# Performance work log

Hardware: AMD Instinct MI355X
Metric: run time of the kernel (lower is better)

## Reference

```python
import jax, jax.numpy as jnp
import numpy as np


def _scan_dir(x, A, B, reverse):
    """First-order linear recurrence h_i = A*h_{i-1} + B*x_i along last axis (W).
    x: [Bsz, C, H, W]; A, B: [C]. reverse=True scans right-to-left but returns
    states in original index order (matching torch scan_backward)."""
    xs = jnp.moveaxis(x, -1, 0)  # [W, Bsz, C, H]
    Ab = A[None, :, None]
    Bb = B[None, :, None]
    def step(h, xi):
        h = Ab * h + Bb * xi
        return h, h
    h0 = jnp.zeros_like(xs[0])
    _, hs = jax.lax.scan(step, h0, xs, reverse=reverse)
    return jnp.moveaxis(hs, 0, -1)  # [Bsz, C, H, W]


def _conv1x1(x, W, b):
    # x: [B,Cin,H,W], W: [Cout,Cin], b: [Cout]
    return jnp.einsum('bchw,dc->bdhw', x, W) + b[None, :, None, None]


def setup_inputs() -> dict:
    key = jax.random.key(0)
    ks = jax.random.split(key, 10)
    B, C, H, W = 8, 64, 128, 128
    D = 128  # hidden_dim
    return {
        'F_in': jax.random.normal(ks[0], (B, C, H, W), dtype=jnp.float32),
        'prior': jax.random.uniform(ks[1], (B, 1, H, W), dtype=jnp.float32),
        'Wi': jax.random.normal(ks[2], (D, C), dtype=jnp.float32) * 0.05,
        'bi': jnp.zeros((D,), dtype=jnp.float32),
        'A_param': jax.random.normal(ks[3], (D,), dtype=jnp.float32),
        'B_param': jax.random.normal(ks[4], (D,), dtype=jnp.float32),
        'alpha': jnp.float32(0.1),
        'gamma': jnp.float32(0.1),
        'Wf': jax.random.normal(ks[5], (D, 4 * D), dtype=jnp.float32) * 0.05,
        'bf': jnp.zeros((D,), dtype=jnp.float32),
        'Wo': jax.random.normal(ks[6], (C, D), dtype=jnp.float32) * 0.05,
        'bo': jnp.zeros((C,), dtype=jnp.float32),
    }


def reference(F_in, prior, Wi, bi, A_param, B_param, alpha, gamma, Wf, bf, Wo, bo):
    # prior has 1 channel, repeated to C channels (prior already matches HxW)
    prior_r = jnp.broadcast_to(prior, F_in.shape)
    F_mod = F_in + alpha * prior_r
    x = _conv1x1(F_mod, Wi, bi)  # [B, D, H, W]
    A = jnp.tanh(A_param)
    Bp = B_param
    h_lr = _scan_dir(x, A, Bp, reverse=False)
    h_rl = _scan_dir(x, A, Bp, reverse=True)
    xt = jnp.swapaxes(x, 2, 3)  # scan over H axis
    h_tb = jnp.swapaxes(_scan_dir(xt, A, Bp, reverse=False), 2, 3)
    h_bt = jnp.swapaxes(_scan_dir(xt, A, Bp, reverse=True), 2, 3)
    h = jnp.concatenate([h_lr, h_rl, h_tb, h_bt], axis=1)  # [B, 4D, H, W]
    h = _conv1x1(h, Wf, bf)   # fusion -> [B, D, H, W]
    out = _conv1x1(h, Wo, bo)  # output_proj -> [B, C, H, W]
    return F_mod + gamma * out
```

## Files before the change

kernel.cpp:

```cpp
#include <hip/hip_runtime.h>
#include <hip/hip_bf16.h>

typedef unsigned int u32;
typedef unsigned short u16;
typedef float f32x2 __attribute__((ext_vector_type(2)));
typedef float f32x4 __attribute__((ext_vector_type(4)));
using bf16x8 = __attribute__((ext_vector_type(8))) short;
using f32x4v = __attribute__((ext_vector_type(4))) float;

#define DEVINL __device__ __forceinline__

constexpr int XTS = 136;
constexpr int XT_BYTES = 128 * XTS * 2;
constexpr int LDS_MAIN = 2 * XT_BYTES;
constexpr int XS = 132;
constexpr int LDS_X = 128 * XS * 2;

DEVINL float bf2f(u16 u) { union { u32 i; float f; } v; v.i = ((u32)u) << 16; return v.f; }
DEVINL u16 f2bf(float f) {
  union { float f; u32 i; } v; v.f = f;
  u32 b = v.i;
  b += 0x7fffu + ((b >> 16) & 1u);
  return (u16)(b >> 16);
}
DEVINL u32 pack2(float a, float b) { return (u32)f2bf(a) | ((u32)f2bf(b) << 16); }

__global__ __launch_bounds__(256) void k_pre(
    const float* __restrict__ Wf, const float* __restrict__ Wo,
    const float* __restrict__ bf_, const float* __restrict__ bo,
    const float* __restrict__ A_param,
    float* __restrict__ A_t, float* __restrict__ beff, u16* __restrict__ Mrow) {
  const int wg = blockIdx.x, t = threadIdx.x;
  if (wg < 128) {
    const int idx = wg * 256 + t;
    const int cout = idx >> 9;
    const int k = idx & 511;
    float s = 0.f;
    for (int d = 0; d < 128; ++d) s = fmaf(Wo[cout * 128 + d], Wf[d * 512 + k], s);
    const int dir = k >> 7, dm = k & 127;
    Mrow[(dir * 64 + cout) * 128 + dm] = f2bf(s);
  } else {
    if (t < 128) A_t[t] = tanhf(A_param[t]);
    if (t < 64) {
      float s = bo[t];
      for (int d = 0; d < 128; ++d) s = fmaf(Wo[t * 128 + d], bf_[d], s);
      beff[t] = s;
    }
  }
}

extern __shared__ char smem[];

DEVINL void load_mfrags(const u16* __restrict__ Mrow, int dir_base, int lane,
                        bf16x8 (&afr)[2][4][4]) {
  const int l15 = lane & 15, kg = lane >> 4;
#pragma unroll
  for (int dir = 0; dir < 2; ++dir)
#pragma unroll
    for (int ct = 0; ct < 4; ++ct)
#pragma unroll
      for (int ks = 0; ks < 4; ++ks)
        afr[dir][ct][ks] = *(const bf16x8*)(
            Mrow + ((size_t)(dir_base + dir) * 64 + ct * 16 + l15) * 128 + ks * 32 + kg * 8);
}

template <bool REV>
DEVINL void scan_col(u16* buf, int d, float A, float Bv) {
  float hv = 0.f;
  float nx[8];
#pragma unroll
  for (int j = 0; j < 8; ++j) {
    const int idx = REV ? (127 - j) : j;
    nx[j] = bf2f(buf[idx * XTS + d]);
  }
  for (int ib = 0; ib < 128; ib += 8) {
    float cur[8];
#pragma unroll
    for (int j = 0; j < 8; ++j) cur[j] = nx[j];
    if (ib + 8 < 128) {
#pragma unroll
      for (int j = 0; j < 8; ++j) {
        const int idx = REV ? (127 - (ib + 8 + j)) : (ib + 8 + j);
        nx[j] = bf2f(buf[idx * XTS + d]);
      }
    }
#pragma unroll
    for (int j = 0; j < 8; ++j) {
      const int idx = REV ? (127 - (ib + j)) : (ib + j);
      hv = fmaf(A, hv, Bv * cur[j]);
      buf[idx * XTS + d] = f2bf(hv);
    }
  }
}

DEVINL void combine_mfma(const u16* H0, const u16* H1, const bf16x8 (&afr)[2][4][4],
                         int t, float* OutS) {
  const int lane = t & 63, wv = t >> 6;
  const int l15 = lane & 15;
  const int kgrp = (lane >> 4) * 16;
  f32x4v acc[4][2];
#pragma unroll
  for (int i = 0; i < 4; ++i)
#pragma unroll
    for (int j = 0; j < 2; ++j) acc[i][j] = (f32x4v)0.f;

#pragma unroll
  for (int dir = 0; dir < 2; ++dir) {
    const u16* Hsrc = dir ? H1 : H0;
#pragma unroll
    for (int ks = 0; ks < 4; ++ks) {
      bf16x8 bfr[2];
#pragma unroll
      for (int pt = 0; pt < 2; ++pt)
        bfr[pt] = *(const bf16x8*)((const char*)Hsrc +
                    (wv * 32 + pt * 16 + l15) * (XTS * 2) + ks * 64 + kgrp);
#pragma unroll
      for (int ct = 0; ct < 4; ++ct)
#pragma unroll
        for (int pt = 0; pt < 2; ++pt)
          acc[ct][pt] = __builtin_amdgcn_mfma_f32_16x16x32_bf16(afr[dir][ct][ks], bfr[pt], acc[ct][pt], 0, 0, 0);
    }
  }
  __syncthreads();
#pragma unroll
  for (int ct = 0; ct < 4; ++ct)
#pragma unroll
    for (int pt = 0; pt < 2; ++pt)
#pragma unroll
      for (int r = 0; r < 4; ++r)
        OutS[(ct * 16 + (lane >> 4) * 4 + r) * 134 + wv * 32 + pt * 16 + l15] = acc[ct][pt][r];
  __syncthreads();
}

__global__ __launch_bounds__(256, 2) void k_horiz(
    const float* __restrict__ F_in, const float* __restrict__ prior,
    const float* __restrict__ Wi, const float* __restrict__ bi,
    const float* __restrict__ Bp, const float* __restrict__ alpha_p,
    const float* __restrict__ A_t, const u16* __restrict__ Mrow,
    u16* __restrict__ x_out, float* __restrict__ out_partial) {
  u16* Xt = (u16*)smem;
  u16* Hl = (u16*)(smem + XT_BYTES);
  char* FT = (char*)Hl;
  float* OutS = (float*)smem;

  const int t = threadIdx.x;
  const int lane = t & 63, wv = t >> 6, l15 = lane & 15, kg = lane >> 4;
  const int bid = blockIdx.x, b = bid >> 7, h = bid & 127;

  bf16x8 bWi[8][2];
#pragma unroll
  for (int nt = 0; nt < 8; ++nt)
#pragma unroll
    for (int ks = 0; ks < 2; ++ks) {
      const float* wp = Wi + (nt * 16 + l15) * 64 + ks * 32 + kg * 8;
      const f32x4 a = *(const f32x4*)(wp);
      const f32x4 c = *(const f32x4*)(wp + 4);
      union { bf16x8 v; uint4 u; } cv;
      cv.u.x = pack2(a.x, a.y);  cv.u.y = pack2(a.z, a.w);
      cv.u.z = pack2(c.x, c.y);  cv.u.w = pack2(c.z, c.w);
      bWi[nt][ks] = cv.v;
    }

  {
    const int w = t & 127, ch = t >> 7;
    const float alpha = alpha_p[0];
    const float pv = prior[(b * 128 + h) * 128 + w];
    const float* Fb = F_in + ((size_t)b * 64 + ch * 32) * 16384 + h * 128 + w;
    const u32 sw = (u32)((w & 7) << 4);
    char* rowp = FT + w * 128;
#pragma unroll
    for (int q = 0; q < 4; ++q) {
      float fv[8];
#pragma unroll
      for (int j = 0; j < 8; ++j) fv[j] = fmaf(alpha, pv, Fb[(q * 8 + j) * 16384]);
      uint4 pk;
      pk.x = pack2(fv[0], fv[1]); pk.y = pack2(fv[2], fv[3]);
      pk.z = pack2(fv[4], fv[5]); pk.w = pack2(fv[6], fv[7]);
      *(uint4*)(rowp + ((ch * 64 + q * 16) ^ sw)) = pk;
    }
  }
  __syncthreads();

  {
    float biv[8];
#pragma unroll
    for (int nt = 0; nt < 8; ++nt) biv[nt] = bi[nt * 16 + l15];

    f32x4v acc[2][8];
#pragma unroll
    for (int i = 0; i < 2; ++i)
#pragma unroll
      for (int j = 0; j < 8; ++j) acc[i][j] = (f32x4v)0.f;

#pragma unroll
    for (int ks = 0; ks < 2; ++ks)
#pragma unroll
      for (int mt = 0; mt < 2; ++mt) {
        const int row = wv * 32 + mt * 16 + l15;
        const bf16x8 aF = *(const bf16x8*)(FT + row * 128 + ((ks * 64 + kg * 16) ^ ((row & 7) << 4)));
#pragma unroll
        for (int nt = 0; nt < 8; ++nt)
          acc[mt][nt] = __builtin_amdgcn_mfma_f32_16x16x32_bf16(aF, bWi[nt][ks], acc[mt][nt], 0, 0, 0);
      }

#pragma unroll
    for (int mt = 0; mt < 2; ++mt)
#pragma unroll
      for (int nt = 0; nt < 8; ++nt)
#pragma unroll
        for (int r = 0; r < 4; ++r) {
          const int w = wv * 32 + mt * 16 + kg * 4 + r;
          Xt[w * XTS + nt * 16 + l15] = f2bf(acc[mt][nt][r] + biv[nt]);
        }
  }
  __syncthreads();

  {
    u16* xg = x_out + (size_t)(b * 128 + h) * 16384;
    for (int i = t; i < 2048; i += 256) {
      const int r = i >> 4, q = i & 15;
      *(uint4*)(xg + r * 128 + q * 8) = *(const uint4*)((const char*)Xt + r * (XTS * 2) + q * 16);
    }
    for (int i = t; i < XT_BYTES / 16; i += 256)
      *(uint4*)((char*)Hl + i * 16) = *(const uint4*)((const char*)Xt + i * 16);
  }

  bf16x8 afr[2][4][4];
  load_mfrags(Mrow, 0, lane, afr);
  __syncthreads();

  {
    const int d = t & 127;
    const float A = A_t[d], Bv = Bp[d];
    if (t < 128) scan_col<false>(Hl, d, A, Bv);
    else         scan_col<true>(Xt, d, A, Bv);
  }
  __syncthreads();

  combine_mfma(Hl, Xt, afr, t, OutS);

  float* og = out_partial + ((size_t)b * 64 * 128 + h) * 128;
  for (int i = t; i < 8192; i += 256) {
    const int c = i >> 7, ww = i & 127;
    og[c * 16384 + ww] = OutS[c * 134 + ww];
  }
}

__global__ __launch_bounds__(256, 2) void k_vert(
    const u16* __restrict__ x_ws, const float* __restrict__ Bp,
    const float* __restrict__ A_t, const u16* __restrict__ Mrow,
    u16* __restrict__ accT) {
  u16* Xv = (u16*)smem;
  u16* Hv = (u16*)(smem + XT_BYTES);
  float* OutS = (float*)smem;

  const int t = threadIdx.x;
  const int lane = t & 63;
  const int bid = blockIdx.x, b = bid >> 7, w = bid & 127;

  for (int i = t; i < 2048; i += 256) {
    const int hh = i >> 4, q = i & 15;
    const uint4 v = *(const uint4*)(x_ws + ((size_t)(b * 128 + hh) * 128 + w) * 128 + q * 8);
    *(uint4*)((char*)Xv + hh * (XTS * 2) + q * 16) = v;
  }
  bf16x8 afr[2][4][4];
  load_mfrags(Mrow, 2, lane, afr);
  __syncthreads();
  for (int i = t; i < XT_BYTES / 16; i += 256)
    *(uint4*)((char*)Hv + i * 16) = *(const uint4*)((const char*)Xv + i * 16);
  __syncthreads();

  {
    const int d = t & 127;
    const float A = A_t[d], Bv = Bp[d];
    if (t < 128) scan_col<false>(Hv, d, A, Bv);
    else         scan_col<true>(Xv, d, A, Bv);
  }
  __syncthreads();

  combine_mfma(Hv, Xv, afr, t, OutS);

  for (int i = t; i < 4096; i += 256) {
    const int c = i >> 6, h2 = (i & 63) * 2;
    const u32 pk = pack2(OutS[c * 134 + h2], OutS[c * 134 + h2 + 1]);
    *(u32*)(accT + ((size_t)(b * 64 + c) * 128 + w) * 128 + h2) = pk;
  }
}

__global__ __launch_bounds__(256) void k_final(
    const float* __restrict__ F_in, const float* __restrict__ prior,
    const float* __restrict__ alpha_p, const float* __restrict__ gamma_p,
    const float* __restrict__ beff, const u16* __restrict__ accT,
    float* __restrict__ out) {
  u16* Xu = (u16*)smem;
  u32* Xw = (u32*)smem;
  const int t = threadIdx.x;
  const int bid = blockIdx.x, b = bid >> 6, c = bid & 63;
  const size_t base = (size_t)bid * 16384;

  for (int i = t; i < 2048; i += 256) {
    const int r = i >> 4, j = i & 15;
    const uint4 v = *(const uint4*)(accT + base + r * 128 + j * 8);
    u32* dst = Xw + r * 66 + j * 4;
    dst[0] = v.x; dst[1] = v.y; dst[2] = v.z; dst[3] = v.w;
  }
  __syncthreads();
  const float alpha = alpha_p[0], gamma = gamma_p[0];
  const float be = beff[c];
  for (int i = t; i < 2048; i += 256) {
    const int hh = i >> 4, w8 = (i & 15) * 8;
    float sv[8];
#pragma unroll
    for (int q = 0; q < 8; ++q) sv[q] = bf2f(Xu[(w8 + q) * XS + hh]);
    const size_t off = base + hh * 128 + w8;
    const float* Fp = F_in + off;
    float* Op = out + off;
    const float* Pp = prior + (b * 128 + hh) * 128 + w8;
#pragma unroll
    for (int q = 0; q < 8; ++q) {
      Op[q] = Fp[q] + alpha * Pp[q] + gamma * (Op[q] + be + sv[q]);
    }
  }
}

extern "C" void kernel_launch(void* const* d_in, const int* in_sizes, int n_in,
                              void* d_out, int out_size, void* d_ws, size_t ws_size,
                              hipStream_t stream) {
  const float* F_in   = (const float*)d_in[0];
  const float* prior  = (const float*)d_in[1];
  const float* Wi     = (const float*)d_in[2];
  const float* bi     = (const float*)d_in[3];
  const float* A_par  = (const float*)d_in[4];
  const float* B_par  = (const float*)d_in[5];
  const float* alpha  = (const float*)d_in[6];
  const float* gamma  = (const float*)d_in[7];
  const float* Wf     = (const float*)d_in[8];
  const float* bf_    = (const float*)d_in[9];
  const float* Wo     = (const float*)d_in[10];
  const float* bo     = (const float*)d_in[11];
  float* out = (float*)d_out;

  char* ws = (char*)d_ws;
  float* A_t   = (float*)ws;
  float* beff  = (float*)(ws + 512);
  u16*   Mrow  = (u16*)(ws + 1024);
  u16*   x_ws  = (u16*)(ws + 66560);
  u16*   accT  = (u16*)(ws + 66560 + 33554432);

  hipFuncSetAttribute((const void*)k_horiz, hipFuncAttributeMaxDynamicSharedMemorySize, LDS_MAIN);
  hipFuncSetAttribute((const void*)k_vert,  hipFuncAttributeMaxDynamicSharedMemorySize, LDS_MAIN);

  k_pre  <<<129, 256, 0, stream>>>(Wf, Wo, bf_, bo, A_par, A_t, beff, Mrow);
  k_horiz<<<1024, 256, LDS_MAIN, stream>>>(F_in, prior, Wi, bi, B_par, alpha, A_t, Mrow, x_ws, out);
  k_vert <<<1024, 256, LDS_MAIN, stream>>>(x_ws, B_par, A_t, Mrow, accT);
  k_final<<<512, 256, LDS_X, stream>>>(F_in, prior, alpha, gamma, beff, accT, out);
}
```

Before: 108.6 us.

## Halve LDS per block, run direction scans sequentially, store horizontal partial as bf16

The horizontal and vertical kernels now use a single LDS buffer instead of two. The forward and reverse scans run one after the other, with the source tile kept in registers and restored between passes, and each scan thread handles a channel pair packed in u32. The horizontal kernel feeds F_in straight into the MFMA A-fragments without an LDS staging pass, and folds the bias into the accumulator init. Its partial output goes to a bf16 workspace instead of fp32 in out, which k_final reads. Launch bounds rise to 4 blocks per CU, trading full-block scan parallelism (only 64 threads scan) and extra barriers for higher occupancy and less memory traffic.

Result: slower. 124.4 us (+14.6%).

```diff
diff --git a/kernel.cpp b/kernel.cpp
--- a/kernel.cpp
+++ b/kernel.cpp
@@ -12,11 +12,12 @@
 
 constexpr int XTS = 136;
 constexpr int XT_BYTES = 128 * XTS * 2;
-constexpr int LDS_MAIN = 2 * XT_BYTES;
 constexpr int XS = 132;
 constexpr int LDS_X = 128 * XS * 2;
 
 DEVINL float bf2f(u16 u) { union { u32 i; float f; } v; v.i = ((u32)u) << 16; return v.f; }
+DEVINL float bf2f_lo(u32 u) { union { u32 i; float f; } v; v.i = u << 16; return v.f; }
+DEVINL float bf2f_hi(u32 u) { union { u32 i; float f; } v; v.i = u & 0xffff0000u; return v.f; }
 DEVINL u16 f2bf(float f) {
   union { float f; u32 i; } v; v.f = f;
   u32 b = v.i;
@@ -51,96 +52,73 @@
 
 extern __shared__ char smem[];
 
-DEVINL void load_mfrags(const u16* __restrict__ Mrow, int dir_base, int lane,
-                        bf16x8 (&afr)[2][4][4]) {
-  const int l15 = lane & 15, kg = lane >> 4;
-#pragma unroll
-  for (int dir = 0; dir < 2; ++dir)
-#pragma unroll
-    for (int ct = 0; ct < 4; ++ct)
-#pragma unroll
-      for (int ks = 0; ks < 4; ++ks)
-        afr[dir][ct][ks] = *(const bf16x8*)(
-            Mrow + ((size_t)(dir_base + dir) * 64 + ct * 16 + l15) * 128 + ks * 32 + kg * 8);
-}
-
 template <bool REV>
-DEVINL void scan_col(u16* buf, int d, float A, float Bv) {
-  float hv = 0.f;
-  float nx[8];
-#pragma unroll
-  for (int j = 0; j < 8; ++j) {
-    const int idx = REV ? (127 - j) : j;
-    nx[j] = bf2f(buf[idx * XTS + d]);
-  }
+DEVINL void scan_pair(u16* buf, int dp, float A0, float A1, float B0, float B1) {
+  float h0 = 0.f, h1 = 0.f;
+  u32* base = (u32*)(buf + dp * 2);
+  constexpr int RS = XTS / 2;
+  u32 nx[8];
+#pragma unroll
+  for (int j = 0; j < 8; ++j) nx[j] = base[(REV ? (127 - j) : j) * RS];
   for (int ib = 0; ib < 128; ib += 8) {
-    float cur[8];
+    u32 cur[8];
 #pragma unroll
     for (int j = 0; j < 8; ++j) cur[j] = nx[j];
     if (ib + 8 < 128) {
 #pragma unroll
       for (int j = 0; j < 8; ++j) {
-        const int idx = REV ? (127 - (ib + 8 + j)) : (ib + 8 + j);
-        nx[j] = bf2f(buf[idx * XTS + d]);
+        const int i = ib + 8 + j;
+        nx[j] = base[(REV ? (127 - i) : i) * RS];
       }
     }
 #pragma unroll
     for (int j = 0; j < 8; ++j) {
-      const int idx = REV ? (127 - (ib + j)) : (ib + j);
-      hv = fmaf(A, hv, Bv * cur[j]);
-      buf[idx * XTS + d] = f2bf(hv);
-    }
-  }
-}
-
-DEVINL void combine_mfma(const u16* H0, const u16* H1, const bf16x8 (&afr)[2][4][4],
-                         int t, float* OutS) {
-  const int lane = t & 63, wv = t >> 6;
-  const int l15 = lane & 15;
-  const int kgrp = (lane >> 4) * 16;
-  f32x4v acc[4][2];
-#pragma unroll
-  for (int i = 0; i < 4; ++i)
-#pragma unroll
-    for (int j = 0; j < 2; ++j) acc[i][j] = (f32x4v)0.f;
-
-#pragma unroll
-  for (int dir = 0; dir < 2; ++dir) {
-    const u16* Hsrc = dir ? H1 : H0;
-#pragma unroll
-    for (int ks = 0; ks < 4; ++ks) {
-      bf16x8 bfr[2];
+      const int i = ib + j;
+      h0 = fmaf(A0, h0, B0 * bf2f_lo(cur[j]));
+      h1 = fmaf(A1, h1, B1 * bf2f_hi(cur[j]));
+      base[(REV ? (127 - i) : i) * RS] = pack2(h0, h1);
+    }
+  }
+}
+
+DEVINL void combine_pass(const u16* Hbuf, const u16* __restrict__ Mrow, int dir,
+                         int lane, int wv, f32x4v (&acc2)[4][2]) {
+  const int l15 = lane & 15, kg = lane >> 4;
+#pragma unroll
+  for (int ks = 0; ks < 4; ++ks) {
+    bf16x8 afr[4], bfr[2];
+#pragma unroll
+    for (int ct = 0; ct < 4; ++ct)
+      afr[ct] = *(const bf16x8*)(Mrow + ((size_t)dir * 64 + ct * 16 + l15) * 128 + ks * 32 + kg * 8);
+#pragma unroll
+    for (int pt = 0; pt < 2; ++pt)
+      bfr[pt] = *(const bf16x8*)((const char*)Hbuf + (wv * 32 + pt * 16 + l15) * (XTS * 2) + ks * 64 + kg * 16);
+#pragma unroll
+    for (int ct = 0; ct < 4; ++ct)
 #pragma unroll
       for (int pt = 0; pt < 2; ++pt)
-        bfr[pt] = *(const bf16x8*)((const char*)Hsrc +
-                    (wv * 32 + pt * 16 + l15) * (XTS * 2) + ks * 64 + kgrp);
-#pragma unroll
-      for (int ct = 0; ct < 4; ++ct)
-#pragma unroll
-        for (int pt = 0; pt < 2; ++pt)
-          acc[ct][pt] = __builtin_amdgcn_mfma_f32_16x16x32_bf16(afr[dir][ct][ks], bfr[pt], acc[ct][pt], 0, 0, 0);
-    }
-  }
-  __syncthreads();
+        acc2[ct][pt] = __builtin_amdgcn_mfma_f32_16x16x32_bf16(afr[ct], bfr[pt], acc2[ct][pt], 0, 0, 0);
+  }
+}
+
+DEVINL void acc_to_outs(const f32x4v (&acc2)[4][2], int lane, int wv, float* OutS) {
+  const int l15 = lane & 15, kg = lane >> 4;
 #pragma unroll
   for (int ct = 0; ct < 4; ++ct)
 #pragma unroll
     for (int pt = 0; pt < 2; ++pt)
 #pragma unroll
       for (int r = 0; r < 4; ++r)
-        OutS[(ct * 16 + (lane >> 4) * 4 + r) * 134 + wv * 32 + pt * 16 + l15] = acc[ct][pt][r];
-  __syncthreads();
-}
-
-__global__ __launch_bounds__(256, 2) void k_horiz(
+        OutS[(ct * 16 + kg * 4 + r) * 134 + wv * 32 + pt * 16 + l15] = acc2[ct][pt][r];
+}
+
+__global__ __launch_bounds__(256, 4) void k_horiz(
     const float* __restrict__ F_in, const float* __restrict__ prior,
     const float* __restrict__ Wi, const float* __restrict__ bi,
     const float* __restrict__ Bp, const float* __restrict__ alpha_p,
     const float* __restrict__ A_t, const u16* __restrict__ Mrow,
-    u16* __restrict__ x_out, float* __restrict__ out_partial) {
-  u16* Xt = (u16*)smem;
-  u16* Hl = (u16*)(smem + XT_BYTES);
-  char* FT = (char*)Hl;
+    u16* __restrict__ x_out, u16* __restrict__ Sh) {
+  u16* buf = (u16*)smem;
   float* OutS = (float*)smem;
 
   const int t = threadIdx.x;
@@ -162,128 +140,175 @@
     }
 
   {
-    const int w = t & 127, ch = t >> 7;
     const float alpha = alpha_p[0];
-    const float pv = prior[(b * 128 + h) * 128 + w];
-    const float* Fb = F_in + ((size_t)b * 64 + ch * 32) * 16384 + h * 128 + w;
-    const u32 sw = (u32)((w & 7) << 4);
-    char* rowp = FT + w * 128;
-#pragma unroll
-    for (int q = 0; q < 4; ++q) {
-      float fv[8];
-#pragma unroll
-      for (int j = 0; j < 8; ++j) fv[j] = fmaf(alpha, pv, Fb[(q * 8 + j) * 16384]);
-      uint4 pk;
-      pk.x = pack2(fv[0], fv[1]); pk.y = pack2(fv[2], fv[3]);
-      pk.z = pack2(fv[4], fv[5]); pk.w = pack2(fv[6], fv[7]);
-      *(uint4*)(rowp + ((ch * 64 + q * 16) ^ sw)) = pk;
-    }
-  }
-  __syncthreads();
-
-  {
-    float biv[8];
-#pragma unroll
-    for (int nt = 0; nt < 8; ++nt) biv[nt] = bi[nt * 16 + l15];
+    float pv[2];
+#pragma unroll
+    for (int mt = 0; mt < 2; ++mt)
+      pv[mt] = prior[(b * 128 + h) * 128 + wv * 32 + mt * 16 + l15];
 
     f32x4v acc[2][8];
 #pragma unroll
-    for (int i = 0; i < 2; ++i)
-#pragma unroll
-      for (int j = 0; j < 8; ++j) acc[i][j] = (f32x4v)0.f;
-
-#pragma unroll
-    for (int ks = 0; ks < 2; ++ks)
+    for (int mt = 0; mt < 2; ++mt)
+#pragma unroll
+      for (int nt = 0; nt < 8; ++nt) {
+        const float bv = bi[nt * 16 + l15];
+        acc[mt][nt] = (f32x4v){ bv, bv, bv, bv };
+      }
+
+#pragma unroll
+    for (int ks = 0; ks < 2; ++ks) {
+      bf16x8 aF[2];
 #pragma unroll
       for (int mt = 0; mt < 2; ++mt) {
-        const int row = wv * 32 + mt * 16 + l15;
-        const bf16x8 aF = *(const bf16x8*)(FT + row * 128 + ((ks * 64 + kg * 16) ^ ((row & 7) << 4)));
+        const int w = wv * 32 + mt * 16 + l15;
+        const float* Fp = F_in + (size_t)b * 1048576 + (size_t)(ks * 32 + kg * 8) * 16384 + h * 128 + w;
+        float fv[8];
+#pragma unroll
+        for (int j = 0; j < 8; ++j) fv[j] = fmaf(alpha, pv[mt], Fp[(size_t)j * 16384]);
+        union { bf16x8 v; uint4 u; } cv;
+        cv.u.x = pack2(fv[0], fv[1]); cv.u.y = pack2(fv[2], fv[3]);
+        cv.u.z = pack2(fv[4], fv[5]); cv.u.w = pack2(fv[6], fv[7]);
+        aF[mt] = cv.v;
+      }
+#pragma unroll
+      for (int mt = 0; mt < 2; ++mt)
 #pragma unroll
         for (int nt = 0; nt < 8; ++nt)
-          acc[mt][nt] = __builtin_amdgcn_mfma_f32_16x16x32_bf16(aF, bWi[nt][ks], acc[mt][nt], 0, 0, 0);
-      }
+          acc[mt][nt] = __builtin_amdgcn_mfma_f32_16x16x32_bf16(aF[mt], bWi[nt][ks], acc[mt][nt], 0, 0, 0);
+    }
 
 #pragma unroll
     for (int mt = 0; mt < 2; ++mt)
 #pragma unroll
       for (int nt = 0; nt < 8; ++nt)
 #pragma unroll
-        for (int r = 0; r < 4; ++r) {
-          const int w = wv * 32 + mt * 16 + kg * 4 + r;
-          Xt[w * XTS + nt * 16 + l15] = f2bf(acc[mt][nt][r] + biv[nt]);
-        }
-  }
-  __syncthreads();
-
+        for (int r = 0; r < 4; ++r)
+          buf[(wv * 32 + mt * 16 + kg * 4 + r) * XTS + nt * 16 + l15] = f2bf(acc[mt][nt][r]);
+  }
+  __syncthreads();
+
+  uint4 rld[8];
   {
     u16* xg = x_out + (size_t)(b * 128 + h) * 16384;
-    for (int i = t; i < 2048; i += 256) {
-      const int r = i >> 4, q = i & 15;
-      *(uint4*)(xg + r * 128 + q * 8) = *(const uint4*)((const char*)Xt + r * (XTS * 2) + q * 16);
-    }
-    for (int i = t; i < XT_BYTES / 16; i += 256)
-      *(uint4*)((char*)Hl + i * 16) = *(const uint4*)((const char*)Xt + i * 16);
-  }
-
-  bf16x8 afr[2][4][4];
-  load_mfrags(Mrow, 0, lane, afr);
-  __syncthreads();
-
-  {
-    const int d = t & 127;
-    const float A = A_t[d], Bv = Bp[d];
-    if (t < 128) scan_col<false>(Hl, d, A, Bv);
-    else         scan_col<true>(Xt, d, A, Bv);
-  }
-  __syncthreads();
-
-  combine_mfma(Hl, Xt, afr, t, OutS);
-
-  float* og = out_partial + ((size_t)b * 64 * 128 + h) * 128;
-  for (int i = t; i < 8192; i += 256) {
-    const int c = i >> 7, ww = i & 127;
-    og[c * 16384 + ww] = OutS[c * 134 + ww];
-  }
-}
-
-__global__ __launch_bounds__(256, 2) void k_vert(
+#pragma unroll
+    for (int j = 0; j < 8; ++j) {
+      const int i = t + j * 256;
+      rld[j] = *(const uint4*)((const char*)buf + (i >> 4) * (XTS * 2) + (i & 15) * 16);
+      *(uint4*)(xg + (i >> 4) * 128 + (i & 15) * 8) = rld[j];
+    }
+  }
+  __syncthreads();
+
+  if (t < 128 && lane < 32) {
+    const int p = wv * 32 + lane;
+    const f32x2 a = *(const f32x2*)(A_t + p * 2);
+    const f32x2 bb = *(const f32x2*)(Bp + p * 2);
+    scan_pair<false>(buf, p, a.x, a.y, bb.x, bb.y);
+  }
+  __syncthreads();
+
+  f32x4v acc2[4][2];
+#pragma unroll
+  for (int i = 0; i < 4; ++i)
+#pragma unroll
+    for (int j = 0; j < 2; ++j) acc2[i][j] = (f32x4v)0.f;
+  combine_pass(buf, Mrow, 0, lane, wv, acc2);
+  __syncthreads();
+
+#pragma unroll
+  for (int j = 0; j < 8; ++j) {
+    const int i = t + j * 256;
+    *(uint4*)((char*)buf + (i >> 4) * (XTS * 2) + (i & 15) * 16) = rld[j];
+  }
+  __syncthreads();
+
+  if (t < 128 && lane < 32) {
+    const int p = wv * 32 + lane;
+    const f32x2 a = *(const f32x2*)(A_t + p * 2);
+    const f32x2 bb = *(const f32x2*)(Bp + p * 2);
+    scan_pair<true>(buf, p, a.x, a.y, bb.x, bb.y);
+  }
+  __syncthreads();
+
+  combine_pass(buf, Mrow, 1, lane, wv, acc2);
+  __syncthreads();
+
+  acc_to_outs(acc2, lane, wv, OutS);
+  __syncthreads();
+
+  u16* sg = Sh + ((size_t)(b * 64) * 128 + h) * 128;
+  for (int i = t; i < 4096; i += 256) {
+    const int c = i >> 6, w2 = (i & 63) * 2;
+    const f32x2 v = *(const f32x2*)(OutS + c * 134 + w2);
+    *(u32*)(sg + (size_t)c * 16384 + w2) = pack2(v.x, v.y);
+  }
+}
+
+__global__ __launch_bounds__(256, 4) void k_vert(
     const u16* __restrict__ x_ws, const float* __restrict__ Bp,
     const float* __restrict__ A_t, const u16* __restrict__ Mrow,
     u16* __restrict__ accT) {
-  u16* Xv = (u16*)smem;
-  u16* Hv = (u16*)(smem + XT_BYTES);
+  u16* buf = (u16*)smem;
   float* OutS = (float*)smem;
 
   const int t = threadIdx.x;
-  const int lane = t & 63;
+  const int lane = t & 63, wv = t >> 6;
   const int bid = blockIdx.x, b = bid >> 7, w = bid & 127;
 
-  for (int i = t; i < 2048; i += 256) {
-    const int hh = i >> 4, q = i & 15;
-    const uint4 v = *(const uint4*)(x_ws + ((size_t)(b * 128 + hh) * 128 + w) * 128 + q * 8);
-    *(uint4*)((char*)Xv + hh * (XTS * 2) + q * 16) = v;
-  }
-  bf16x8 afr[2][4][4];
-  load_mfrags(Mrow, 2, lane, afr);
-  __syncthreads();
-  for (int i = t; i < XT_BYTES / 16; i += 256)
-    *(uint4*)((char*)Hv + i * 16) = *(const uint4*)((const char*)Xv + i * 16);
-  __syncthreads();
-
-  {
-    const int d = t & 127;
-    const float A = A_t[d], Bv = Bp[d];
-    if (t < 128) scan_col<false>(Hv, d, A, Bv);
-    else         scan_col<true>(Xv, d, A, Bv);
-  }
-  __syncthreads();
-
-  combine_mfma(Hv, Xv, afr, t, OutS);
+  uint4 rld[8];
+#pragma unroll
+  for (int j = 0; j < 8; ++j) {
+    const int i = t + j * 256;
+    rld[j] = *(const uint4*)(x_ws + ((size_t)(b * 128 + (i >> 4)) * 128 + w) * 128 + (i & 15) * 8);
+  }
+#pragma unroll
+  for (int j = 0; j < 8; ++j) {
+    const int i = t + j * 256;
+    *(uint4*)((char*)buf + (i >> 4) * (XTS * 2) + (i & 15) * 16) = rld[j];
+  }
+  __syncthreads();
+
+  if (t < 128 && lane < 32) {
+    const int p = wv * 32 + lane;
+    const f32x2 a = *(const f32x2*)(A_t + p * 2);
+    const f32x2 bb = *(const f32x2*)(Bp + p * 2);
+    scan_pair<false>(buf, p, a.x, a.y, bb.x, bb.y);
+  }
+  __syncthreads();
+
+  f32x4v acc2[4][2];
+#pragma unroll
+  for (int i = 0; i < 4; ++i)
+#pragma unroll
+    for (int j = 0; j < 2; ++j) acc2[i][j] = (f32x4v)0.f;
+  combine_pass(buf, Mrow, 2, lane, wv, acc2);
+  __syncthreads();
+
+#pragma unroll
+  for (int j = 0; j < 8; ++j) {
+    const int i = t + j * 256;
+    *(uint4*)((char*)buf + (i >> 4) * (XTS * 2) + (i & 15) * 16) = rld[j];
+  }
+  __syncthreads();
+
+  if (t < 128 && lane < 32) {
+    const int p = wv * 32 + lane;
+    const f32x2 a = *(const f32x2*)(A_t + p * 2);
+    const f32x2 bb = *(const f32x2*)(Bp + p * 2);
+    scan_pair<true>(buf, p, a.x, a.y, bb.x, bb.y);
+  }
+  __syncthreads();
+
+  combine_pass(buf, Mrow, 3, lane, wv, acc2);
+  __syncthreads();
+
+  acc_to_outs(acc2, lane, wv, OutS);
+  __syncthreads();
 
   for (int i = t; i < 4096; i += 256) {
     const int c = i >> 6, h2 = (i & 63) * 2;
-    const u32 pk = pack2(OutS[c * 134 + h2], OutS[c * 134 + h2 + 1]);
-    *(u32*)(accT + ((size_t)(b * 64 + c) * 128 + w) * 128 + h2) = pk;
+    const f32x2 v = *(const f32x2*)(OutS + c * 134 + h2);
+    *(u32*)(accT + ((size_t)(b * 64 + c) * 128 + w) * 128 + h2) = pack2(v.x, v.y);
   }
 }
 
@@ -291,7 +316,7 @@
     const float* __restrict__ F_in, const float* __restrict__ prior,
     const float* __restrict__ alpha_p, const float* __restrict__ gamma_p,
     const float* __restrict__ beff, const u16* __restrict__ accT,
-    float* __restrict__ out) {
+    const u16* __restrict__ Sh, float* __restrict__ out) {
   u16* Xu = (u16*)smem;
   u32* Xw = (u32*)smem;
   const int t = threadIdx.x;
@@ -314,11 +339,14 @@
     for (int q = 0; q < 8; ++q) sv[q] = bf2f(Xu[(w8 + q) * XS + hh]);
     const size_t off = base + hh * 128 + w8;
     const float* Fp = F_in + off;
+    const u16* Sp = Sh + off;
     float* Op = out + off;
     const float* Pp = prior + (b * 128 + hh) * 128 + w8;
+    const uint4 sh4 = *(const uint4*)(Sp);
+    const u16* sh8 = (const u16*)&sh4;
 #pragma unroll
     for (int q = 0; q < 8; ++q) {
-      Op[q] = Fp[q] + alpha * Pp[q] + gamma * (Op[q] + be + sv[q]);
+      Op[q] = Fp[q] + alpha * Pp[q] + gamma * (bf2f(sh8[q]) + be + sv[q]);
     }
   }
 }
@@ -345,13 +373,14 @@
   float* beff  = (float*)(ws + 512);
   u16*   Mrow  = (u16*)(ws + 1024);
   u16*   x_ws  = (u16*)(ws + 66560);
-  u16*   accT  = (u16*)(ws + 66560 + 33554432);
-
-  hipFuncSetAttribute((const void*)k_horiz, hipFuncAttributeMaxDynamicSharedMemorySize, LDS_MAIN);
-  hipFuncSetAttribute((const void*)k_vert,  hipFuncAttributeMaxDynamicSharedMemorySize, LDS_MAIN);
+  u16*   Sh_ws = (u16*)(ws + 66560 + 33554432);
+  u16*   accT  = (u16*)(ws + 66560 + 50331648);
+
+  hipFuncSetAttribute((const void*)k_horiz, hipFuncAttributeMaxDynamicSharedMemorySize, XT_BYTES);
+  hipFuncSetAttribute((const void*)k_vert,  hipFuncAttributeMaxDynamicSharedMemorySize, XT_BYTES);
 
   k_pre  <<<129, 256, 0, stream>>>(Wf, Wo, bf_, bo, A_par, A_t, beff, Mrow);
-  k_horiz<<<1024, 256, LDS_MAIN, stream>>>(F_in, prior, Wi, bi, B_par, alpha, A_t, Mrow, x_ws, out);
-  k_vert <<<1024, 256, LDS_MAIN, stream>>>(x_ws, B_par, A_t, Mrow, accT);
-  k_final<<<512, 256, LDS_X, stream>>>(F_in, prior, alpha, gamma, beff, accT, out);
-}
+  k_horiz<<<1024, 256, XT_BYTES, stream>>>(F_in, prior, Wi, bi, B_par, alpha, A_t, Mrow, x_ws, Sh_ws);
+  k_vert <<<1024, 256, XT_BYTES, stream>>>(x_ws, B_par, A_t, Mrow, accT);
+  k_final<<<512, 256, LDS_X, stream>>>(F_in, prior, alpha, gamma, beff, accT, Sh_ws, out);
+}
```
